# Performance work log

Measured on AMD Instinct MI355X. Metric: run time of the kernel, lower is better.

Reference implementation:

```python
import jax, jax.numpy as jnp
import numpy as np

N_NODES = 50000
N_EDGES = 1600000
IN_CH = 128
HID = 32
HEADS = 3
OUT_CH = 32
NEG_SLOPE = 0.2


def setup_inputs() -> dict:
    key = jax.random.key(0)
    ks = jax.random.split(key, 12)
    s = 0.05
    x = jax.random.normal(ks[0], (N_NODES, IN_CH), dtype=jnp.float32)
    edge_index = jax.random.randint(ks[1], (2, N_EDGES), 0, N_NODES, dtype=jnp.int64)
    W1 = jax.random.normal(ks[2], (IN_CH, HEADS * HID), dtype=jnp.float32) * s
    att_src1 = jax.random.normal(ks[3], (HEADS, HID), dtype=jnp.float32) * s
    att_dst1 = jax.random.normal(ks[4], (HEADS, HID), dtype=jnp.float32) * s
    b1 = jnp.zeros((HEADS * HID,), dtype=jnp.float32)
    W2 = jax.random.normal(ks[5], (HEADS * HID, OUT_CH), dtype=jnp.float32) * s
    att_src2 = jax.random.normal(ks[6], (1, OUT_CH), dtype=jnp.float32) * s
    att_dst2 = jax.random.normal(ks[7], (1, OUT_CH), dtype=jnp.float32) * s
    b2 = jnp.zeros((OUT_CH,), dtype=jnp.float32)
    Wp = jax.random.normal(ks[8], (OUT_CH, 1), dtype=jnp.float32) * s
    bp = jnp.zeros((1,), dtype=jnp.float32)
    return dict(x=x, edge_index=edge_index, W1=W1, att_src1=att_src1,
                att_dst1=att_dst1, b1=b1, W2=W2, att_src2=att_src2,
                att_dst2=att_dst2, b2=b2, Wp=Wp, bp=bp)


def gat_layer(x, src, dst, W, a_src, a_dst, b, heads, out_ch, concat):
    # PyG GATConv semantics: per-head linear, edge attention with leaky_relu,
    # softmax over incoming edges per destination node, scatter-add aggregate.
    N = x.shape[0]
    h = (x @ W).reshape(N, heads, out_ch)                 # [N,H,C]
    a_s = jnp.einsum('nhc,hc->nh', h, a_src)              # [N,H]
    a_d = jnp.einsum('nhc,hc->nh', h, a_dst)              # [N,H]
    e = jax.nn.leaky_relu(a_s[src] + a_d[dst], NEG_SLOPE) # [E,H]
    m = jax.ops.segment_max(e, dst, num_segments=N)       # stable softmax per dst
    p = jnp.exp(e - m[dst])
    s = jax.ops.segment_sum(p, dst, num_segments=N)
    alpha = p / (s[dst] + 1e-16)                          # [E,H]
    msg = h[src] * alpha[:, :, None]                      # [E,H,C]
    out = jax.ops.segment_sum(msg, dst, num_segments=N)   # [N,H,C]
    out = out.reshape(N, heads * out_ch) if concat else out.mean(axis=1)
    return out + b


def reference(x, edge_index, W1, att_src1, att_dst1, b1, W2, att_src2,
              att_dst2, b2, Wp, bp):
    N = x.shape[0]
    loop = jnp.arange(N, dtype=edge_index.dtype)
    src = jnp.concatenate([edge_index[0], loop])  # add self-loops (PyG default)
    dst = jnp.concatenate([edge_index[1], loop])
    h = gat_layer(x, src, dst, W1, att_src1, att_dst1, b1, HEADS, HID, True)
    h = jax.nn.elu(h)
    h = gat_layer(h, src, dst, W2, att_src2, att_dst2, b2, 1, OUT_CH, False)
    prob = jax.nn.sigmoid(h @ Wp + bp)                    # [N,1]
    return prob
```

## Files before the change

### kernel.cpp

```cpp
#include <hip/hip_runtime.h>
#include <hip/hip_bf16.h>
#include <math.h>


#define IN_CH 128
#define HID 32
#define HEADS 3
#define OUT_CH 32
#define NEG_SLOPE 0.2f

#define NBUCK_SHIFT 6
#define NBUCK_NODES 64
#define BCAP 2560
#define EPB 4096

typedef unsigned int uint;
typedef unsigned short ushort;
typedef short v8s __attribute__((ext_vector_type(8)));
typedef float v4f __attribute__((ext_vector_type(4)));

static __device__ __forceinline__ uint f2bf(float f) {
    uint u = __float_as_uint(f);
    return (u + 0x7FFFu + ((u >> 16) & 1u)) >> 16;
}
static __device__ __forceinline__ uint pk4fp8(float a, float b, float c, float d) {
    int r = 0;
    r = __builtin_amdgcn_cvt_pk_fp8_f32(a, b, r, false);
    r = __builtin_amdgcn_cvt_pk_fp8_f32(c, d, r, true);
    return (uint)r;
}
static __device__ __forceinline__ float elu_f(float o) {
    return o > 0.f ? o : __expf(o) - 1.f;
}
static __device__ __forceinline__ float frcp(float x) {
    return __builtin_amdgcn_rcpf(x);
}

#define LDA 136
#define LDC 100


__global__ __launch_bounds__(256) void k_g1b(const float* __restrict__ x,
                                             const float* __restrict__ W1,
                                             const float* __restrict__ as,
                                             const float* __restrict__ ad,
                                             uint* __restrict__ h1u,
                                             float* __restrict__ a_d1p,
                                             const int* __restrict__ ei,
                                             int E, int Etot, int B2, int G1,
                                             int* __restrict__ gcur,
                                             uint* __restrict__ stage, int N) {
    __shared__ __attribute__((aligned(16))) char raw[(64 * LDA + 96 * LDA) * 2];
    int tid = threadIdx.x;

    if ((int)blockIdx.x >= G1) {
        int* hist     = (int*)raw;
        int* runStart = hist + 1024;
        int* rankCtr  = runStart + 1024;
        for (int i = tid; i < 1024; i += 256) { hist[i] = 0; rankCtr[i] = 0; }
        __syncthreads();
        int base = ((int)blockIdx.x - G1) * EPB;

        uint rec[16];
        #pragma unroll
        for (int i = 0; i < 16; ++i) {
            int e = base + tid + i * 256;
            uint r = 0xFFFFFFFFu;
            if (e < Etot) {
                int s, d;
                if (e < E) { s = ei[e]; d = ei[E + e]; }
                else       { s = e - E; d = s; }
                r = ((uint)d << 16) | (uint)s;
                atomicAdd(&hist[d >> NBUCK_SHIFT], 1);
            }
            rec[i] = r;
        }
        __syncthreads();
        for (int i = tid; i < B2; i += 256) {
            int c = hist[i];
            if (c) runStart[i] = atomicAdd(&gcur[i], c);
        }
        __syncthreads();
        #pragma unroll
        for (int i = 0; i < 16; ++i) {
            uint r = rec[i];
            if (r != 0xFFFFFFFFu) {
                int b = (int)(r >> 16) >> NBUCK_SHIFT;
                int pos = runStart[b] + atomicAdd(&rankCtr[b], 1);
                if (pos < BCAP)
                    stage[(size_t)b * BCAP + pos] = r & 0x003FFFFFu;
            }
        }
        return;
    }

    ushort* sA  = (ushort*)raw;
    ushort* sBT = sA + 64 * LDA;
    float*  sC  = (float*)raw;
    int b0 = blockIdx.x * 64;

    uint* sA32 = (uint*)sA;
    #pragma unroll
    for (int i = 0; i < 8; ++i) {
        int g = tid + i * 256;
        int row = g >> 5, c4 = g & 31;
        float4 v = make_float4(0.f, 0.f, 0.f, 0.f);
        int gn = b0 + row;
        if (gn < N) v = *(const float4*)(x + (size_t)gn * IN_CH + c4 * 4);
        sA32[row * 68 + c4 * 2]     = f2bf(v.x) | (f2bf(v.y) << 16);
        sA32[row * 68 + c4 * 2 + 1] = f2bf(v.z) | (f2bf(v.w) << 16);
    }
    #pragma unroll
    for (int i = 0; i < 12; ++i) {
        int g = tid + i * 256;
        int k = g / 24, c4 = (g - k * 24) * 4;
        float4 v = *(const float4*)(W1 + k * 96 + c4);
        sBT[(c4 + 0) * LDA + k] = (ushort)f2bf(v.x);
        sBT[(c4 + 1) * LDA + k] = (ushort)f2bf(v.y);
        sBT[(c4 + 2) * LDA + k] = (ushort)f2bf(v.z);
        sBT[(c4 + 3) * LDA + k] = (ushort)f2bf(v.w);
    }
    __syncthreads();

    int l = tid & 63, w = tid >> 6;
    int m15 = l & 15, q = l >> 4;

    v8s afr[4];
    const ushort* arow = sA + (w * 16 + m15) * LDA + q * 8;
    #pragma unroll
    for (int kc = 0; kc < 4; ++kc) afr[kc] = *(const v8s*)(arow + kc * 32);

    v4f acc[6];
    #pragma unroll
    for (int cg = 0; cg < 6; ++cg) {
        acc[cg] = (v4f){0.f, 0.f, 0.f, 0.f};
        const ushort* brow = sBT + (cg * 16 + m15) * LDA + q * 8;
        #pragma unroll
        for (int kc = 0; kc < 4; ++kc) {
            v8s bfr = *(const v8s*)(brow + kc * 32);
            acc[cg] = __builtin_amdgcn_mfma_f32_16x16x32_bf16(afr[kc], bfr, acc[cg], 0, 0, 0);
        }
    }
    __syncthreads();
    #pragma unroll
    for (int cg = 0; cg < 6; ++cg) {
        int col = cg * 16 + m15;
        #pragma unroll
        for (int r = 0; r < 4; ++r)
            sC[(w * 16 + q * 4 + r) * LDC + col] = acc[cg][r];
    }
    __syncthreads();

    if (tid < 192) {
        int ln = tid / 3, h = tid - ln * 3;
        int node = b0 + ln;
        if (node < N) {
            const float* vs = as + h * 32;
            const float* vd = ad + h * 32;
            const float* row = sC + ln * LDC + h * 32;
            float s = 0.f, d = 0.f;
            #pragma unroll
            for (int c = 0; c < 32; ++c) { float v = row[c]; s += v * vs[c]; d += v * vd[c]; }
            ((float*)h1u)[(size_t)node * 32 + 24 + h] = s;
            a_d1p[node * 4 + h] = d;
        }
    }
    {
        int node = tid >> 2, part = tid & 3;
        int gn = b0 + node;
        if (gn < N) {
            const float* row = sC + node * LDC + part * 24;
            uint tmp[6];
            #pragma unroll
            for (int j = 0; j < 6; ++j)
                tmp[j] = pk4fp8(row[4*j], row[4*j+1], row[4*j+2], row[4*j+3]);
            uint* dst = h1u + (size_t)gn * 32 + part * 6;
            *(uint2*)(dst + 0) = make_uint2(tmp[0], tmp[1]);
            *(uint2*)(dst + 2) = make_uint2(tmp[2], tmp[3]);
            *(uint2*)(dst + 4) = make_uint2(tmp[4], tmp[5]);
        }
    }
}


__global__ __launch_bounds__(256) void k_sort(const uint* __restrict__ stage,
                                              const int* __restrict__ gcur,
                                              int* __restrict__ offs,
                                              uint* __restrict__ edges,
                                              int N, int Etot, int B2) {
    __shared__ uint items[BCAP];
    __shared__ int red[256];
    __shared__ int lofs[NBUCK_NODES + 1];
    __shared__ int cursors[NBUCK_NODES];
    int t = threadIdx.x;
    int b = blockIdx.x;

    int partial = 0;
    for (int i = t; i < b; i += 256) partial += gcur[i];
    red[t] = partial;
    if (t < NBUCK_NODES) cursors[t] = 0;
    __syncthreads();
    #pragma unroll
    for (int s = 128; s > 0; s >>= 1) {
        if (t < s) red[t] += red[t + s];
        __syncthreads();
    }
    int gbase = red[0];
    int cnt = gcur[b]; if (cnt > BCAP) cnt = BCAP;

    for (int i = t; i < cnt; i += 256) items[i] = stage[(size_t)b * BCAP + i];
    __syncthreads();
    for (int i = t; i < cnt; i += 256) atomicAdd(&cursors[items[i] >> 16], 1);
    __syncthreads();
    if (t == 0) {
        int run = 0;
        for (int i = 0; i < NBUCK_NODES; ++i) { int v = cursors[i]; lofs[i] = run; run += v; }
        lofs[NBUCK_NODES] = run;
    }
    __syncthreads();
    int nodeBase = b << NBUCK_SHIFT;
    if (t < NBUCK_NODES && nodeBase + t < N) offs[nodeBase + t] = gbase + lofs[t];
    if (b == B2 - 1 && t == 0) offs[N] = Etot;
    if (t < NBUCK_NODES) cursors[t] = 0;
    __syncthreads();
    uint addHi = (uint)nodeBase << 16;
    for (int i = t; i < cnt; i += 256) {
        uint it = items[i];
        int ln = (int)(it >> 16);
        int r = atomicAdd(&cursors[ln], 1);
        edges[gbase + lofs[ln] + r] = it + addHi;
    }
}


#define W2LD 36

#define A1_GATHER(EIDX, AF, W0, W1, W2)                                        \
    {                                                                          \
        uint pk = edges[EIDX];                                                 \
        uint src = pk & 0xFFFFu;                                               \
        const uint* hr = h1u + src * 32u;                                      \
        AF = *(const float4*)(hr + 24);                                        \
        W0 = hr[d]; W1 = hr[d + 8]; W2 = hr[d + 16];                           \
    }

#define A1_COMPUTE(AF, W0, W1, W2)                                             \
    {                                                                          \
        float z0 = AF.x + adv.x, z1 = AF.y + adv.y, z2 = AF.z + adv.z;         \
        z0 = fmaxf(z0, NEG_SLOPE * z0);                                        \
        z1 = fmaxf(z1, NEG_SLOPE * z1);                                        \
        z2 = fmaxf(z2, NEG_SLOPE * z2);                                        \
        float p0 = __expf(z0), p1 = __expf(z1), p2 = __expf(z2);               \
        { auto lo = __builtin_amdgcn_cvt_pk_f32_fp8((int)W0, false);           \
          auto hi = __builtin_amdgcn_cvt_pk_f32_fp8((int)W0, true);            \
          a00 += p0 * lo[0]; a01 += p0 * lo[1];                                \
          a02 += p0 * hi[0]; a03 += p0 * hi[1]; }                              \
        { auto lo = __builtin_amdgcn_cvt_pk_f32_fp8((int)W1, false);           \
          auto hi = __builtin_amdgcn_cvt_pk_f32_fp8((int)W1, true);            \
          a10 += p1 * lo[0]; a11 += p1 * lo[1];                                \
          a12 += p1 * hi[0]; a13 += p1 * hi[1]; }                              \
        { auto lo = __builtin_amdgcn_cvt_pk_f32_fp8((int)W2, false);           \
          auto hi = __builtin_amdgcn_cvt_pk_f32_fp8((int)W2, true);            \
          a20 += p2 * lo[0]; a21 += p2 * lo[1];                                \
          a22 += p2 * hi[0]; a23 += p2 * hi[1]; }                              \
        d0 += p0; d1 += p1; d2 += p2;                                          \
    }

__global__ __launch_bounds__(256) void k_agg1g2(const int* __restrict__ offs,
                                                const uint* __restrict__ edges,
                                                const uint* __restrict__ h1u,
                                                const float* __restrict__ a_d1p,
                                                const float* __restrict__ b1,
                                                const float* __restrict__ W2,
                                                const float* __restrict__ as2,
                                                const float* __restrict__ ad2,
                                                uint* __restrict__ h2u,
                                                float* __restrict__ a_d2, int N) {
    __shared__ __attribute__((aligned(16))) float sW2[96 * W2LD];
    __shared__ float ss2[32], sd2[32];
    __shared__ float rowbuf[4][96];

    int tid = threadIdx.x;
    #pragma unroll
    for (int i = 0; i < 3; ++i) {
        int g = tid + i * 256;
        int k = g >> 3, c4i = g & 7;
        *(float4*)&sW2[k * W2LD + c4i * 4] = *(const float4*)(W2 + k * 32 + c4i * 4);
    }
    if (tid < 32) { ss2[tid] = as2[tid]; sd2[tid] = ad2[tid]; }
    __syncthreads();

    int w = tid >> 6;
    int node = blockIdx.x * 4 + w;
    if (node >= N) return;
    int lane = tid & 63;
    int g = lane >> 3, d = lane & 7;
    const float4 adv = *(const float4*)(a_d1p + node * 4);

    int off0 = offs[node], off1 = offs[node + 1];
    int deg = off1 - off0;
    if (deg < 0) deg = 0;
    float a00 = 0.f, a01 = 0.f, a02 = 0.f, a03 = 0.f;
    float a10 = 0.f, a11 = 0.f, a12 = 0.f, a13 = 0.f;
    float a20 = 0.f, a21 = 0.f, a22 = 0.f, a23 = 0.f;
    float d0 = 0.f, d1 = 0.f, d2 = 0.f;

    int nf = deg >> 3;
    {
        float4 afA = make_float4(0.f, 0.f, 0.f, 0.f);
        float4 afB = make_float4(0.f, 0.f, 0.f, 0.f);
        uint wA0 = 0, wA1 = 0, wA2 = 0, wB0 = 0, wB1 = 0, wB2 = 0;
        int i = 0;
        if (nf > 0) A1_GATHER((uint)(off0 + g),     afA, wA0, wA1, wA2)
        if (nf > 1) A1_GATHER((uint)(off0 + 8 + g), afB, wB0, wB1, wB2)
        for (; i + 3 < nf; i += 2) {
            A1_COMPUTE(afA, wA0, wA1, wA2)
            A1_GATHER((uint)(off0 + (i + 2) * 8 + g), afA, wA0, wA1, wA2)
            A1_COMPUTE(afB, wB0, wB1, wB2)
            A1_GATHER((uint)(off0 + (i + 3) * 8 + g), afB, wB0, wB1, wB2)
        }
        if (i < nf) {
            bool more  = (i + 1 < nf);
            bool third = (i + 2 < nf);
            A1_COMPUTE(afA, wA0, wA1, wA2)
            if (third) A1_GATHER((uint)(off0 + (i + 2) * 8 + g), afA, wA0, wA1, wA2)
            if (more)  A1_COMPUTE(afB, wB0, wB1, wB2)
            if (third) A1_COMPUTE(afA, wA0, wA1, wA2)
        }
    }
    if (g < (deg & 7)) {
        float4 afT; uint wT0, wT1, wT2;
        A1_GATHER((uint)(off0 + nf * 8 + g), afT, wT0, wT1, wT2)
        A1_COMPUTE(afT, wT0, wT1, wT2)
    }

    #define REDF(v) { v += __shfl_xor(v, 8); v += __shfl_xor(v, 16); v += __shfl_xor(v, 32); }
    REDF(a00) REDF(a01) REDF(a02) REDF(a03)
    REDF(a10) REDF(a11) REDF(a12) REDF(a13)
    REDF(a20) REDF(a21) REDF(a22) REDF(a23)
    REDF(d0) REDF(d1) REDF(d2)
    #undef REDF

    if (lane < 8) {
        float r0 = frcp(d0 + 1e-16f);
        float r1 = frcp(d1 + 1e-16f);
        float r2 = frcp(d2 + 1e-16f);
        float4 bv0 = *(const float4*)(b1 + 4 * lane);
        float4 bv1 = *(const float4*)(b1 + 32 + 4 * lane);
        float4 bv2 = *(const float4*)(b1 + 64 + 4 * lane);
        float4 v;
        v.x = elu_f(a00 * r0 + bv0.x);
        v.y = elu_f(a01 * r0 + bv0.y);
        v.z = elu_f(a02 * r0 + bv0.z);
        v.w = elu_f(a03 * r0 + bv0.w);
        *(float4*)&rowbuf[w][4 * lane] = v;
        v.x = elu_f(a10 * r1 + bv1.x);
        v.y = elu_f(a11 * r1 + bv1.y);
        v.z = elu_f(a12 * r1 + bv1.z);
        v.w = elu_f(a13 * r1 + bv1.w);
        *(float4*)&rowbuf[w][32 + 4 * lane] = v;
        v.x = elu_f(a20 * r2 + bv2.x);
        v.y = elu_f(a21 * r2 + bv2.y);
        v.z = elu_f(a22 * r2 + bv2.z);
        v.w = elu_f(a23 * r2 + bv2.w);
        *(float4*)&rowbuf[w][64 + 4 * lane] = v;
    }

    int c4 = lane & 7, kg = lane >> 3;
    float4 accv = make_float4(0.f, 0.f, 0.f, 0.f);
    const float* rb = &rowbuf[w][kg * 12];
    const float* wb = &sW2[kg * 12 * W2LD + c4 * 4];
    #pragma unroll 12
    for (int i = 0; i < 12; ++i) {
        float rv = rb[i];
        float4 wv = *(const float4*)(wb + i * W2LD);
        accv.x += rv * wv.x; accv.y += rv * wv.y;
        accv.z += rv * wv.z; accv.w += rv * wv.w;
    }
    #define REDF(c) { c += __shfl_xor(c, 8); c += __shfl_xor(c, 16); c += __shfl_xor(c, 32); }
    REDF(accv.x) REDF(accv.y) REDF(accv.z) REDF(accv.w)
    #undef REDF

    float4 sv = *(const float4*)&ss2[c4 * 4];
    float4 dv = *(const float4*)&sd2[c4 * 4];
    float ps = accv.x * sv.x + accv.y * sv.y + accv.z * sv.z + accv.w * sv.w;
    float pd = accv.x * dv.x + accv.y * dv.y + accv.z * dv.z + accv.w * dv.w;
    ps += __shfl_xor(ps, 1); ps += __shfl_xor(ps, 2); ps += __shfl_xor(ps, 4);
    pd += __shfl_xor(pd, 1); pd += __shfl_xor(pd, 2); pd += __shfl_xor(pd, 4);
    if (lane < 8) {
        h2u[(size_t)node * 16 + c4] = pk4fp8(accv.x, accv.y, accv.z, accv.w);
        if (lane == 0) {
            ((float*)h2u)[(size_t)node * 16 + 8] = ps;
            a_d2[node] = pd;
        }
    }
}


#define A2_GATHER(EIDX, ZF, WV)                                                \
    {                                                                          \
        uint pk = edges[EIDX];                                                 \
        uint src = pk & 0xFFFFu;                                               \
        const uint* hr = h2u + src * 16u;                                      \
        ZF = *(const float*)(hr + 8);                                          \
        WV = hr[d];                                                            \
    }

#define A2_COMPUTE(ZF, WV)                                                     \
    {                                                                          \
        float z = ZF + ad2u;                                                   \
        z = fmaxf(z, NEG_SLOPE * z);                                           \
        float p = __expf(z);                                                   \
        auto lo = __builtin_amdgcn_cvt_pk_f32_fp8((int)WV, false);             \
        auto hi = __builtin_amdgcn_cvt_pk_f32_fp8((int)WV, true);              \
        c0 += p * lo[0]; c1 += p * lo[1];                                      \
        c2 += p * hi[0]; c3 += p * hi[1];                                      \
        den += p;                                                              \
    }

__global__ __launch_bounds__(256) void k_agg2f(const int* __restrict__ offs,
                                               const uint* __restrict__ edges,
                                               const uint* __restrict__ h2u,
                                               const float* __restrict__ a_d2,
                                               const float* __restrict__ b2,
                                               const float* __restrict__ Wp,
                                               const float* __restrict__ bp,
                                               float* __restrict__ out, int N) {
    int node = blockIdx.x * 4 + (threadIdx.x >> 6);
    if (node >= N) return;
    int lane = threadIdx.x & 63;
    int g = lane >> 3, d = lane & 7;
    const float ad2u = a_d2[node];

    int off0 = offs[node], off1 = offs[node + 1];
    int deg = off1 - off0;
    if (deg < 0) deg = 0;
    float c0 = 0.f, c1 = 0.f, c2 = 0.f, c3 = 0.f, den = 0.f;

    int nf = deg >> 3;
    {
        float zA = 0.f, zB = 0.f; uint vA = 0, vB = 0;
        int i = 0;
        if (nf > 0) A2_GATHER((uint)(off0 + g),     zA, vA)
        if (nf > 1) A2_GATHER((uint)(off0 + 8 + g), zB, vB)
        for (; i + 3 < nf; i += 2) {
            A2_COMPUTE(zA, vA)
            A2_GATHER((uint)(off0 + (i + 2) * 8 + g), zA, vA)
            A2_COMPUTE(zB, vB)
            A2_GATHER((uint)(off0 + (i + 3) * 8 + g), zB, vB)
        }
        if (i < nf) {
            bool more  = (i + 1 < nf);
            bool third = (i + 2 < nf);
            A2_COMPUTE(zA, vA)
            if (third) A2_GATHER((uint)(off0 + (i + 2) * 8 + g), zA, vA)
            if (more)  A2_COMPUTE(zB, vB)
            if (third) A2_COMPUTE(zA, vA)
        }
    }
    if (g < (deg & 7)) {
        float zT; uint vT;
        A2_GATHER((uint)(off0 + nf * 8 + g), zT, vT)
        A2_COMPUTE(zT, vT)
    }

    #define REDF(v) { v += __shfl_xor(v, 8); v += __shfl_xor(v, 16); v += __shfl_xor(v, 32); }
    REDF(c0) REDF(c1) REDF(c2) REDF(c3) REDF(den)
    #undef REDF

    float4 bv = *(const float4*)(b2 + 4 * d);
    float4 wv = *(const float4*)(Wp + 4 * d);
    float r = frcp(den + 1e-16f);
    float v = (c0 * r + bv.x) * wv.x + (c1 * r + bv.y) * wv.y +
              (c2 * r + bv.z) * wv.z + (c3 * r + bv.w) * wv.w;
    v += __shfl_xor(v, 1);
    v += __shfl_xor(v, 2);
    v += __shfl_xor(v, 4);
    if (lane == 0)
        out[node] = frcp(1.f + __expf(-(v + bp[0])));
}


extern "C" void kernel_launch(void* const* d_in, const int* in_sizes, int n_in,
                              void* d_out, int out_size, void* d_ws, size_t ws_size,
                              hipStream_t stream) {
    const float* x      = (const float*)d_in[0];
    const int*   ei     = (const int*)d_in[1];
    const float* W1     = (const float*)d_in[2];
    const float* att_s1 = (const float*)d_in[3];
    const float* att_d1 = (const float*)d_in[4];
    const float* b1     = (const float*)d_in[5];
    const float* W2     = (const float*)d_in[6];
    const float* att_s2 = (const float*)d_in[7];
    const float* att_d2 = (const float*)d_in[8];
    const float* b2     = (const float*)d_in[9];
    const float* Wp     = (const float*)d_in[10];
    const float* bp     = (const float*)d_in[11];
    float* out = (float*)d_out;

    const int N = in_sizes[0] / IN_CH;
    const int E = in_sizes[1] / 2;
    const int Etot = E + N;
    const int B2 = (N + NBUCK_NODES - 1) >> NBUCK_SHIFT;
    const int G1 = (N + 63) / 64;
    const int BK = (Etot + EPB - 1) / EPB;

    float* ws    = (float*)d_ws;
    uint*  h1u   = (uint*)ws;
    float* a_d1p = ws + (size_t)N * 32;
    int*   offs  = (int*)(a_d1p + (size_t)N * 4);
    uint*  edges = (uint*)(offs + (N + 1));
    int*   gcur  = (int*)(edges + Etot);
    uint*  stage = (uint*)(gcur + 1024);
    uint*  h2u   = stage + (size_t)B2 * BCAP;
    float* a_d2  = (float*)(h2u + (size_t)N * 16);

    (void)hipMemsetAsync(gcur, 0, 1024 * sizeof(int), stream);

    k_g1b<<<G1 + BK, 256, 0, stream>>>(x, W1, att_s1, att_d1, h1u, a_d1p,
                                       ei, E, Etot, B2, G1, gcur, stage, N);
    k_sort<<<B2, 256, 0, stream>>>(stage, gcur, offs, edges, N, Etot, B2);

    k_agg1g2<<<(N + 3) / 4, 256, 0, stream>>>(offs, edges, h1u, a_d1p, b1, W2,
                                              att_s2, att_d2, h2u, a_d2, N);
    k_agg2f<<<(N + 3) / 4, 256, 0, stream>>>(offs, edges, h2u, a_d2,
                                             b2, Wp, bp, out, N);
}
```

Before: 226.9 us.

## Store sorted edge sources as 16-bit and interleave fp8 head rows for vector gathers

Sorted edge entries are now stored as 16-bit source indices instead of 32-bit packed words, which halves edge-list traffic in both aggregation kernels. The fp8 layer-1 feature rows are reordered so that the three head words a lane needs sit next to each other, letting each gather use a single 12-byte vector load instead of three scalar loads. This relies on node ids fitting in 16 bits (N = 50000), and it drops the destination bits from each entry, which the aggregation kernels did not use.

```diff
diff --git a/kernel.cpp b/kernel.cpp
--- a/kernel.cpp
+++ b/kernel.cpp
@@ -18,6 +18,7 @@
 typedef unsigned short ushort;
 typedef short v8s __attribute__((ext_vector_type(8)));
 typedef float v4f __attribute__((ext_vector_type(4)));
+typedef uint v3u __attribute__((ext_vector_type(3)));
 
 static __device__ __forceinline__ uint f2bf(float f) {
     uint u = __float_as_uint(f);
@@ -169,11 +170,15 @@
         int node = tid >> 2, part = tid & 3;
         int gn = b0 + node;
         if (gn < N) {
-            const float* row = sC + node * LDC + part * 24;
+            const float* row = sC + node * LDC;
             uint tmp[6];
             #pragma unroll
-            for (int j = 0; j < 6; ++j)
-                tmp[j] = pk4fp8(row[4*j], row[4*j+1], row[4*j+2], row[4*j+3]);
+            for (int jj = 0; jj < 6; ++jj) {
+                int j = part * 6 + jj;
+                int dd = j / 3, slot = j - dd * 3;
+                const float* p = row + slot * 32 + dd * 4;
+                tmp[jj] = pk4fp8(p[0], p[1], p[2], p[3]);
+            }
             uint* dst = h1u + (size_t)gn * 32 + part * 6;
             *(uint2*)(dst + 0) = make_uint2(tmp[0], tmp[1]);
             *(uint2*)(dst + 2) = make_uint2(tmp[2], tmp[3]);
@@ -186,7 +191,7 @@
 __global__ __launch_bounds__(256) void k_sort(const uint* __restrict__ stage,
                                               const int* __restrict__ gcur,
                                               int* __restrict__ offs,
-                                              uint* __restrict__ edges,
+                                              ushort* __restrict__ edges,
                                               int N, int Etot, int B2) {
     __shared__ uint items[BCAP];
     __shared__ int red[256];
@@ -223,51 +228,49 @@
     if (b == B2 - 1 && t == 0) offs[N] = Etot;
     if (t < NBUCK_NODES) cursors[t] = 0;
     __syncthreads();
-    uint addHi = (uint)nodeBase << 16;
     for (int i = t; i < cnt; i += 256) {
         uint it = items[i];
         int ln = (int)(it >> 16);
         int r = atomicAdd(&cursors[ln], 1);
-        edges[gbase + lofs[ln] + r] = it + addHi;
+        edges[gbase + lofs[ln] + r] = (ushort)(it & 0xFFFFu);
     }
 }
 
 
 #define W2LD 36
 
-#define A1_GATHER(EIDX, AF, W0, W1, W2)                                        \
+#define A1_GATHER(EIDX, AF, WV)                                                \
     {                                                                          \
-        uint pk = edges[EIDX];                                                 \
-        uint src = pk & 0xFFFFu;                                               \
+        uint src = (uint)edges[EIDX];                                          \
         const uint* hr = h1u + src * 32u;                                      \
         AF = *(const float4*)(hr + 24);                                        \
-        W0 = hr[d]; W1 = hr[d + 8]; W2 = hr[d + 16];                           \
-    }
-
-#define A1_COMPUTE(AF, W0, W1, W2)                                             \
+        WV = *(const v3u*)(hr + 3 * d);                                        \
+    }
+
+#define A1_COMPUTE(AF, WV)                                                     \
     {                                                                          \
         float z0 = AF.x + adv.x, z1 = AF.y + adv.y, z2 = AF.z + adv.z;         \
         z0 = fmaxf(z0, NEG_SLOPE * z0);                                        \
         z1 = fmaxf(z1, NEG_SLOPE * z1);                                        \
         z2 = fmaxf(z2, NEG_SLOPE * z2);                                        \
         float p0 = __expf(z0), p1 = __expf(z1), p2 = __expf(z2);               \
-        { auto lo = __builtin_amdgcn_cvt_pk_f32_fp8((int)W0, false);           \
-          auto hi = __builtin_amdgcn_cvt_pk_f32_fp8((int)W0, true);            \
+        { auto lo = __builtin_amdgcn_cvt_pk_f32_fp8((int)WV[0], false);        \
+          auto hi = __builtin_amdgcn_cvt_pk_f32_fp8((int)WV[0], true);         \
           a00 += p0 * lo[0]; a01 += p0 * lo[1];                                \
           a02 += p0 * hi[0]; a03 += p0 * hi[1]; }                              \
-        { auto lo = __builtin_amdgcn_cvt_pk_f32_fp8((int)W1, false);           \
-          auto hi = __builtin_amdgcn_cvt_pk_f32_fp8((int)W1, true);            \
+        { auto lo = __builtin_amdgcn_cvt_pk_f32_fp8((int)WV[1], false);        \
+          auto hi = __builtin_amdgcn_cvt_pk_f32_fp8((int)WV[1], true);         \
           a10 += p1 * lo[0]; a11 += p1 * lo[1];                                \
           a12 += p1 * hi[0]; a13 += p1 * hi[1]; }                              \
-        { auto lo = __builtin_amdgcn_cvt_pk_f32_fp8((int)W2, false);           \
-          auto hi = __builtin_amdgcn_cvt_pk_f32_fp8((int)W2, true);            \
+        { auto lo = __builtin_amdgcn_cvt_pk_f32_fp8((int)WV[2], false);        \
+          auto hi = __builtin_amdgcn_cvt_pk_f32_fp8((int)WV[2], true);         \
           a20 += p2 * lo[0]; a21 += p2 * lo[1];                                \
           a22 += p2 * hi[0]; a23 += p2 * hi[1]; }                              \
         d0 += p0; d1 += p1; d2 += p2;                                          \
     }
 
 __global__ __launch_bounds__(256) void k_agg1g2(const int* __restrict__ offs,
-                                                const uint* __restrict__ edges,
+                                                const ushort* __restrict__ edges,
                                                 const uint* __restrict__ h1u,
                                                 const float* __restrict__ a_d1p,
                                                 const float* __restrict__ b1,
@@ -309,29 +312,29 @@
     {
         float4 afA = make_float4(0.f, 0.f, 0.f, 0.f);
         float4 afB = make_float4(0.f, 0.f, 0.f, 0.f);
-        uint wA0 = 0, wA1 = 0, wA2 = 0, wB0 = 0, wB1 = 0, wB2 = 0;
+        v3u wA = (v3u){0, 0, 0}, wB = (v3u){0, 0, 0};
         int i = 0;
-        if (nf > 0) A1_GATHER((uint)(off0 + g),     afA, wA0, wA1, wA2)
-        if (nf > 1) A1_GATHER((uint)(off0 + 8 + g), afB, wB0, wB1, wB2)
+        if (nf > 0) A1_GATHER((uint)(off0 + g),     afA, wA)
+        if (nf > 1) A1_GATHER((uint)(off0 + 8 + g), afB, wB)
         for (; i + 3 < nf; i += 2) {
-            A1_COMPUTE(afA, wA0, wA1, wA2)
-            A1_GATHER((uint)(off0 + (i + 2) * 8 + g), afA, wA0, wA1, wA2)
-            A1_COMPUTE(afB, wB0, wB1, wB2)
-            A1_GATHER((uint)(off0 + (i + 3) * 8 + g), afB, wB0, wB1, wB2)
+            A1_COMPUTE(afA, wA)
+            A1_GATHER((uint)(off0 + (i + 2) * 8 + g), afA, wA)
+            A1_COMPUTE(afB, wB)
+            A1_GATHER((uint)(off0 + (i + 3) * 8 + g), afB, wB)
         }
         if (i < nf) {
             bool more  = (i + 1 < nf);
             bool third = (i + 2 < nf);
-            A1_COMPUTE(afA, wA0, wA1, wA2)
-            if (third) A1_GATHER((uint)(off0 + (i + 2) * 8 + g), afA, wA0, wA1, wA2)
-            if (more)  A1_COMPUTE(afB, wB0, wB1, wB2)
-            if (third) A1_COMPUTE(afA, wA0, wA1, wA2)
+            A1_COMPUTE(afA, wA)
+            if (third) A1_GATHER((uint)(off0 + (i + 2) * 8 + g), afA, wA)
+            if (more)  A1_COMPUTE(afB, wB)
+            if (third) A1_COMPUTE(afA, wA)
         }
     }
     if (g < (deg & 7)) {
-        float4 afT; uint wT0, wT1, wT2;
-        A1_GATHER((uint)(off0 + nf * 8 + g), afT, wT0, wT1, wT2)
-        A1_COMPUTE(afT, wT0, wT1, wT2)
+        float4 afT; v3u wT;
+        A1_GATHER((uint)(off0 + nf * 8 + g), afT, wT)
+        A1_COMPUTE(afT, wT)
     }
 
     #define REDF(v) { v += __shfl_xor(v, 8); v += __shfl_xor(v, 16); v += __shfl_xor(v, 32); }
@@ -399,8 +402,7 @@
 
 #define A2_GATHER(EIDX, ZF, WV)                                                \
     {                                                                          \
-        uint pk = edges[EIDX];                                                 \
-        uint src = pk & 0xFFFFu;                                               \
+        uint src = (uint)edges[EIDX];                                          \
         const uint* hr = h2u + src * 16u;                                      \
         ZF = *(const float*)(hr + 8);                                          \
         WV = hr[d];                                                            \
@@ -419,7 +421,7 @@
     }
 
 __global__ __launch_bounds__(256) void k_agg2f(const int* __restrict__ offs,
-                                               const uint* __restrict__ edges,
+                                               const ushort* __restrict__ edges,
                                                const uint* __restrict__ h2u,
                                                const float* __restrict__ a_d2,
                                                const float* __restrict__ b2,
@@ -505,15 +507,15 @@
     const int G1 = (N + 63) / 64;
     const int BK = (Etot + EPB - 1) / EPB;
 
-    float* ws    = (float*)d_ws;
-    uint*  h1u   = (uint*)ws;
-    float* a_d1p = ws + (size_t)N * 32;
-    int*   offs  = (int*)(a_d1p + (size_t)N * 4);
-    uint*  edges = (uint*)(offs + (N + 1));
-    int*   gcur  = (int*)(edges + Etot);
-    uint*  stage = (uint*)(gcur + 1024);
-    uint*  h2u   = stage + (size_t)B2 * BCAP;
-    float* a_d2  = (float*)(h2u + (size_t)N * 16);
+    float*  ws    = (float*)d_ws;
+    uint*   h1u   = (uint*)ws;
+    float*  a_d1p = ws + (size_t)N * 32;
+    int*    offs  = (int*)(a_d1p + (size_t)N * 4);
+    ushort* edges = (ushort*)(offs + (N + 1));
+    int*    gcur  = (int*)(edges + (((size_t)Etot + 1) & ~(size_t)1));
+    uint*   stage = (uint*)(gcur + 1024);
+    uint*   h2u   = stage + (size_t)B2 * BCAP;
+    float*  a_d2  = (float*)(h2u + (size_t)N * 16);
 
     (void)hipMemsetAsync(gcur, 0, 1024 * sizeof(int), stream);
 
```

New measurement: 223.3 us. Within noise of the previous version (-1.6%).
